# Performance work log

Hardware: AMD Instinct MI355X
Metric: run time of the kernel (lower is better)

Reference implementation:

```python
import jax, jax.numpy as jnp
import numpy as np

N = 100000   # nodes
E = 1600000  # edges
B = 128      # graphs
VOCAB, EMB, HID = 10000, 128, 128


def gcn_conv(x, src, dst, ew, W, b, n_nodes):
    # PyG GCNConv: x' = D^{-1/2}(A_w + I) D^{-1/2} (x W) + b, self-loop weight 1
    x = x @ W  # [N, H]
    loop = jnp.arange(n_nodes)
    src2 = jnp.concatenate([src, loop])
    dst2 = jnp.concatenate([dst, loop])
    ew2 = jnp.concatenate([ew, jnp.ones((n_nodes,), x.dtype)])
    deg = jax.ops.segment_sum(ew2, dst2, num_segments=n_nodes)
    dinv = jnp.where(deg > 0, deg ** -0.5, 0.0)
    norm = dinv[src2] * ew2 * dinv[dst2]                      # [E+N]
    msg = x[src2] * norm[:, None]                             # gather-scale
    out = jax.ops.segment_sum(msg, dst2, num_segments=n_nodes)  # scatter-add
    return out + b


def setup_inputs() -> dict:
    key = jax.random.key(0)
    ks = jax.random.split(key, 12)
    x_idx = jax.random.randint(ks[0], (N,), 0, VOCAB)
    edge_index = jax.random.randint(ks[1], (2, E), 0, N)
    edge_weight = jax.random.uniform(ks[2], (E,), jnp.float32)
    batch = jnp.sort(jax.random.randint(ks[3], (N,), 0, B))
    emb_table = jax.random.normal(ks[4], (VOCAB, EMB), jnp.float32)
    emb_table = emb_table.at[0].set(0.0)  # padding_idx=0
    s = 1.0 / np.sqrt(EMB)
    W1 = jax.random.uniform(ks[5], (EMB, HID), jnp.float32, -s, s)
    b1 = jnp.zeros((HID,), jnp.float32)
    W2 = jax.random.uniform(ks[6], (HID, HID), jnp.float32, -s, s)
    b2 = jnp.zeros((HID,), jnp.float32)
    mlp_W1 = jax.random.uniform(ks[7], (HID, HID // 2), jnp.float32, -s, s)
    mlp_b1 = jax.random.uniform(ks[8], (HID // 2,), jnp.float32, -s, s)
    s2 = 1.0 / np.sqrt(HID // 2)
    mlp_W2 = jax.random.uniform(ks[9], (HID // 2, 2), jnp.float32, -s2, s2)
    mlp_b2 = jax.random.uniform(ks[10], (2,), jnp.float32, -s2, s2)
    return dict(x_idx=x_idx, edge_index=edge_index, edge_weight=edge_weight,
                batch=batch, emb_table=emb_table, W1=W1, b1=b1, W2=W2, b2=b2,
                mlp_W1=mlp_W1, mlp_b1=mlp_b1, mlp_W2=mlp_W2, mlp_b2=mlp_b2)


def reference(x_idx, edge_index, edge_weight, batch, emb_table, W1, b1, W2, b2,
              mlp_W1, mlp_b1, mlp_W2, mlp_b2):
    src, dst = edge_index[0], edge_index[1]
    x = emb_table[x_idx]                                  # embedding lookup
    x = jax.nn.relu(gcn_conv(x, src, dst, edge_weight, W1, b1, N))
    # dropout is inference no-op
    x = jax.nn.relu(gcn_conv(x, src, dst, edge_weight, W2, b2, N))
    # global mean pool over graphs
    sums = jax.ops.segment_sum(x, batch, num_segments=B)
    cnts = jax.ops.segment_sum(jnp.ones((N,), x.dtype), batch, num_segments=B)
    g = sums / jnp.maximum(cnts, 1.0)[:, None]            # [B, HID]
    h = jax.nn.relu(g @ mlp_W1 + mlp_b1)
    out = h @ mlp_W2 + mlp_b2
    return jax.nn.softmax(out, axis=1)
```

## Files before the change

### kernel.cpp

```cpp
#include <hip/hip_runtime.h>
#include <hip/hip_bf16.h>

#define NN 100000
#define NE 1600000
#define NB 128
#define NV 10000
#define HD 128

#define NBUCK 782
#define EBLK 512
#define EPB (NE / EBLK)

using bf16x8 = __attribute__((ext_vector_type(8))) short;
using f32x4  = __attribute__((ext_vector_type(4))) float;
typedef __attribute__((ext_vector_type(8))) unsigned short ushortv8;
typedef __attribute__((ext_vector_type(8))) unsigned char ucharv8;
typedef float f32x2 __attribute__((ext_vector_type(2)));

__device__ __forceinline__ float bf2f(unsigned short b) {
  return __uint_as_float((unsigned)b << 16);
}
__device__ __forceinline__ unsigned short f2bf(float f) {
  __hip_bfloat16 h = __float2bfloat16(f);
  return *reinterpret_cast<unsigned short*>(&h);
}
__device__ __forceinline__ unsigned char f2fp8(float f) {
  return (unsigned char)(__builtin_amdgcn_cvt_pk_fp8_f32(f, 0.f, 0, false) & 0xff);
}
__device__ __forceinline__ unsigned packSN(unsigned s, float v) {
  return (s << 15) | ((unsigned)f2bf(v) & 0x7fffu);
}
__device__ __forceinline__ float unpackN(unsigned u) {
  return __uint_as_float((u & 0x7fffu) << 16);
}
__device__ __forceinline__ void acc16(float* acc, uint4 u, float c) {
  f32x2 v;
  v = __builtin_amdgcn_cvt_pk_f32_fp8((int)u.x, false); acc[0] += c*v[0]; acc[1] += c*v[1];
  v = __builtin_amdgcn_cvt_pk_f32_fp8((int)u.x, true);  acc[2] += c*v[0]; acc[3] += c*v[1];
  v = __builtin_amdgcn_cvt_pk_f32_fp8((int)u.y, false); acc[4] += c*v[0]; acc[5] += c*v[1];
  v = __builtin_amdgcn_cvt_pk_f32_fp8((int)u.y, true);  acc[6] += c*v[0]; acc[7] += c*v[1];
  v = __builtin_amdgcn_cvt_pk_f32_fp8((int)u.z, false); acc[8] += c*v[0]; acc[9] += c*v[1];
  v = __builtin_amdgcn_cvt_pk_f32_fp8((int)u.z, true);  acc[10]+= c*v[0]; acc[11]+= c*v[1];
  v = __builtin_amdgcn_cvt_pk_f32_fp8((int)u.w, false); acc[12]+= c*v[0]; acc[13]+= c*v[1];
  v = __builtin_amdgcn_cvt_pk_f32_fp8((int)u.w, true);  acc[14]+= c*v[0]; acc[15]+= c*v[1];
}


__global__ __launch_bounds__(1024) void k_bcount(const int* __restrict__ dst,
                                                 int* __restrict__ cntmat) {
  __shared__ int h[NBUCK];
  int t = threadIdx.x, blk = blockIdx.x;
  for (int i = t; i < NBUCK; i += 1024) h[i] = 0;
  __syncthreads();
  int base = blk * EPB;
  for (int i = t; i < EPB; i += 1024) atomicAdd(&h[dst[base + i] >> 7], 1);
  __syncthreads();
  for (int i = t; i < NBUCK; i += 1024) cntmat[(size_t)blk * NBUCK + i] = h[i];
}

__global__ __launch_bounds__(256) void k_cscan(int* __restrict__ cntmat,
                                               int* __restrict__ totals) {
  __shared__ int sh[256];
  int bu = blockIdx.x, t = threadIdx.x;
  int v0 = cntmat[(size_t)(2 * t) * NBUCK + bu];
  int v1 = cntmat[(size_t)(2 * t + 1) * NBUCK + bu];
  int s = v0 + v1;
  sh[t] = s;
  __syncthreads();
  #pragma unroll
  for (int off = 1; off < 256; off <<= 1) {
    int u = (t >= off) ? sh[t - off] : 0;
    __syncthreads();
    sh[t] += u;
    __syncthreads();
  }
  int pre = sh[t] - s;
  cntmat[(size_t)(2 * t) * NBUCK + bu] = pre;
  cntmat[(size_t)(2 * t + 1) * NBUCK + bu] = pre + v0;
  if (t == 255) totals[bu] = sh[255];
}

__global__ __launch_bounds__(1024) void k_tscan(const int* __restrict__ totals,
                                                int* __restrict__ bucketBase) {
  __shared__ int sh[1024];
  int t = threadIdx.x;
  int v = (t < NBUCK) ? totals[t] : 0;
  sh[t] = v;
  __syncthreads();
  #pragma unroll
  for (int off = 1; off < 1024; off <<= 1) {
    int u = (t >= off) ? sh[t - off] : 0;
    __syncthreads();
    sh[t] += u;
    __syncthreads();
  }
  if (t < NBUCK) bucketBase[t] = sh[t] - v;
  if (t == NBUCK - 1) bucketBase[NBUCK] = sh[t];
}

__global__ __launch_bounds__(1024) void k_bscatter(const int* __restrict__ src,
                                                   const int* __restrict__ dst,
                                                   const float* __restrict__ ew,
                                                   const int* __restrict__ cntmat,
                                                   const int* __restrict__ bucketBase,
                                                   uint2* __restrict__ spair) {
  __shared__ int off[NBUCK];
  int t = threadIdx.x, blk = blockIdx.x;
  for (int i = t; i < NBUCK; i += 1024)
    off[i] = bucketBase[i] + cntmat[(size_t)blk * NBUCK + i];
  __syncthreads();
  int base = blk * EPB;
  for (int i = t; i < EPB; i += 1024) {
    int e = base + i;
    int d = dst[e];
    unsigned pew = packSN((unsigned)src[e], ew[e]);
    int pos = atomicAdd(&off[d >> 7], 1);
    spair[pos] = make_uint2(pew, (unsigned)(d & 127));
  }
}

__global__ __launch_bounds__(256) void k_bdeg(const uint2* __restrict__ spair,
                                              const int* __restrict__ bucketBase,
                                              int* __restrict__ rowptr,
                                              float* __restrict__ dinv) {
  __shared__ int cnt[128];
  __shared__ float ws[128];
  __shared__ int sh[128];
  int bu = blockIdx.x, t = threadIdx.x;
  if (t < 128) { cnt[t] = 0; ws[t] = 0.f; }
  __syncthreads();
  int ebeg = bucketBase[bu], eend = bucketBase[bu + 1];
  for (int e = ebeg + t; e < eend; e += 256) {
    uint2 p = spair[e];
    atomicAdd(&cnt[p.y], 1);
    atomicAdd(&ws[p.y], unpackN(p.x));
  }
  __syncthreads();
  int v = 0;
  if (t < 128) { v = cnt[t]; sh[t] = v; }
  __syncthreads();
  #pragma unroll
  for (int off = 1; off < 128; off <<= 1) {
    int u = 0;
    if (t < 128 && t >= off) u = sh[t - off];
    __syncthreads();
    if (t < 128) sh[t] += u;
    __syncthreads();
  }
  if (t < 128) {
    int gid = (bu << 7) + t;
    if (gid < NN) {
      rowptr[gid] = ebeg + sh[t] - v;
      dinv[gid] = rsqrtf(1.0f + ws[t]);
    }
    if (gid == NN) rowptr[NN] = NE;
  }
}

__global__ __launch_bounds__(256) void k_bfill(const uint2* __restrict__ spair,
                                               const int* __restrict__ bucketBase,
                                               const int* __restrict__ rowptr,
                                               const float* __restrict__ dinv,
                                               unsigned* __restrict__ csr) {
  __shared__ int cnt[128];
  __shared__ float sdv[128];
  __shared__ int srp[128];
  int bu = blockIdx.x, t = threadIdx.x;
  if (t < 128) {
    cnt[t] = 0;
    int gid = (bu << 7) + t;
    if (gid < NN) { sdv[t] = dinv[gid]; srp[t] = rowptr[gid]; }
  }
  __syncthreads();
  int ebeg = bucketBase[bu], eend = bucketBase[bu + 1];
  for (int e = ebeg + t; e < eend; e += 256) {
    uint2 p = spair[e];
    int dl = (int)p.y;
    unsigned s = p.x >> 15;
    float ewf = unpackN(p.x);
    int r = atomicAdd(&cnt[dl], 1);
    float nrm = dinv[s] * ewf * sdv[dl];
    csr[srp[dl] + r] = packSN(s, nrm);
  }
}

__global__ void k_wprep2(const float* __restrict__ W1, const float* __restrict__ W2,
                         unsigned short* __restrict__ Wt1, unsigned short* __restrict__ Wt2) {
  int t = blockIdx.x * blockDim.x + threadIdx.x;
  const float* W = (t < 16384) ? W1 : W2;
  unsigned short* Wt = (t < 16384) ? Wt1 : Wt2;
  int i = t & 16383;
  int k = i >> 7, n = i & 127;
  Wt[n * 128 + k] = f2bf(W[k * 128 + n]);
}

template <bool AF32>
__global__ __launch_bounds__(256) void k_gemm_mfma(const void* __restrict__ Av,
                                                   const unsigned short* __restrict__ Wt,
                                                   unsigned char* __restrict__ C, int M) {
  __shared__ unsigned char Cs[128][132];
  const int t = threadIdx.x;
  const int wave = t >> 6, lane = t & 63;
  const int lrow = lane & 15, lk = lane >> 4;
  const int row0 = blockIdx.x * 128;
  const int wrow = row0 + wave * 32;

  f32x4 acc[2][8];
  #pragma unroll
  for (int i = 0; i < 2; ++i)
    #pragma unroll
    for (int j = 0; j < 8; ++j) acc[i][j] = (f32x4){0.f, 0.f, 0.f, 0.f};

  #pragma unroll
  for (int kt = 0; kt < 4; ++kt) {
    bf16x8 a[2];
    #pragma unroll
    for (int rt = 0; rt < 2; ++rt) {
      int r = wrow + rt * 16 + lrow;
      bf16x8 av = (bf16x8){0, 0, 0, 0, 0, 0, 0, 0};
      if (r < M) {
        if (AF32) {
          const float* ap = (const float*)Av + (size_t)r * HD + kt * 32 + lk * 8;
          #pragma unroll
          for (int j = 0; j < 8; ++j) av[j] = (short)f2bf(ap[j]);
        } else {
          av = *(const bf16x8*)((const unsigned short*)Av + (size_t)r * HD + kt * 32 + lk * 8);
        }
      }
      a[rt] = av;
    }
    #pragma unroll
    for (int ct = 0; ct < 8; ++ct) {
      bf16x8 b = *(const bf16x8*)(Wt + (size_t)(ct * 16 + lrow) * HD + kt * 32 + lk * 8);
      acc[0][ct] = __builtin_amdgcn_mfma_f32_16x16x32_bf16(a[0], b, acc[0][ct], 0, 0, 0);
      acc[1][ct] = __builtin_amdgcn_mfma_f32_16x16x32_bf16(a[1], b, acc[1][ct], 0, 0, 0);
    }
  }

  #pragma unroll
  for (int rt = 0; rt < 2; ++rt)
    #pragma unroll
    for (int ct = 0; ct < 8; ++ct)
      #pragma unroll
      for (int reg = 0; reg < 4; ++reg) {
        int lr = wave * 32 + rt * 16 + lk * 4 + reg;
        Cs[lr][ct * 16 + lrow] = f2fp8(acc[rt][ct][reg]);
      }
  __syncthreads();

  #pragma unroll
  for (int i = 0; i < 8; ++i) {
    int idx = t + i * 256;
    int r = idx >> 4;
    int c = (idx & 15) * 8;
    int gr = row0 + r;
    if (gr < M)
      *(ucharv8*)(C + (size_t)gr * HD + c) = *(const ucharv8*)&Cs[r][c];
  }
}

template <bool IND, bool POOL>
__global__ __launch_bounds__(256) void k_agg8(const unsigned char* __restrict__ xw,
                                              const int* __restrict__ xidx,
                                              const int* __restrict__ rowptr,
                                              const unsigned* __restrict__ csr,
                                              const float* __restrict__ dinv,
                                              const float* __restrict__ bias,
                                              unsigned short* __restrict__ outp,
                                              const int* __restrict__ batch,
                                              float* __restrict__ sums) {
  int t = threadIdx.x;
  int n = blockIdx.x * 32 + (t >> 3);
  int lane = t & 7;
  int beg = rowptr[n], end = rowptr[n + 1];

  int sn = IND ? xidx[n] : n;
  uint4 uself = *(const uint4*)(xw + (size_t)sn * HD + lane * 16);

  float acc[16];
  #pragma unroll
  for (int j = 0; j < 16; ++j) acc[j] = 0.f;

  int e = beg;
  int alignEnd = min(end, (beg + 3) & ~3);
  for (; e < alignEnd; ++e) {
    unsigned u = csr[e];
    int s0 = (int)(u >> 15);
    if (IND) s0 = xidx[s0];
    float c0 = unpackN(u);
    uint4 u0 = *(const uint4*)(xw + (size_t)s0 * HD + lane * 16);
    acc16(acc, u0, c0);
  }
  for (; e + 3 < end; e += 4) {
    uint4 q = *(const uint4*)(csr + e);
    int s0 = (int)(q.x >> 15), s1 = (int)(q.y >> 15);
    int s2 = (int)(q.z >> 15), s3 = (int)(q.w >> 15);
    if (IND) { s0 = xidx[s0]; s1 = xidx[s1]; s2 = xidx[s2]; s3 = xidx[s3]; }
    float c0 = unpackN(q.x), c1 = unpackN(q.y);
    float c2 = unpackN(q.z), c3 = unpackN(q.w);
    uint4 u0 = *(const uint4*)(xw + (size_t)s0 * HD + lane * 16);
    uint4 u1 = *(const uint4*)(xw + (size_t)s1 * HD + lane * 16);
    uint4 u2 = *(const uint4*)(xw + (size_t)s2 * HD + lane * 16);
    uint4 u3 = *(const uint4*)(xw + (size_t)s3 * HD + lane * 16);
    acc16(acc, u0, c0); acc16(acc, u1, c1);
    acc16(acc, u2, c2); acc16(acc, u3, c3);
  }
  for (; e < end; ++e) {
    unsigned u = csr[e];
    int s0 = (int)(u >> 15);
    if (IND) s0 = xidx[s0];
    float c0 = unpackN(u);
    uint4 u0 = *(const uint4*)(xw + (size_t)s0 * HD + lane * 16);
    acc16(acc, u0, c0);
  }

  float d = dinv[n];
  acc16(acc, uself, d * d);

  const float4* bp = reinterpret_cast<const float4*>(bias + lane * 16);
  float4 b0 = bp[0], b1 = bp[1], b2 = bp[2], b3 = bp[3];
  float o[16];
  o[0]  = fmaxf(acc[0]  + b0.x, 0.f); o[1]  = fmaxf(acc[1]  + b0.y, 0.f);
  o[2]  = fmaxf(acc[2]  + b0.z, 0.f); o[3]  = fmaxf(acc[3]  + b0.w, 0.f);
  o[4]  = fmaxf(acc[4]  + b1.x, 0.f); o[5]  = fmaxf(acc[5]  + b1.y, 0.f);
  o[6]  = fmaxf(acc[6]  + b1.z, 0.f); o[7]  = fmaxf(acc[7]  + b1.w, 0.f);
  o[8]  = fmaxf(acc[8]  + b2.x, 0.f); o[9]  = fmaxf(acc[9]  + b2.y, 0.f);
  o[10] = fmaxf(acc[10] + b2.z, 0.f); o[11] = fmaxf(acc[11] + b2.w, 0.f);
  o[12] = fmaxf(acc[12] + b3.x, 0.f); o[13] = fmaxf(acc[13] + b3.y, 0.f);
  o[14] = fmaxf(acc[14] + b3.z, 0.f); o[15] = fmaxf(acc[15] + b3.w, 0.f);

  if constexpr (!POOL) {
    ushortv8 r0, r1;
    #pragma unroll
    for (int j = 0; j < 8; ++j) { r0[j] = f2bf(o[j]); r1[j] = f2bf(o[8 + j]); }
    *(ushortv8*)(outp + (size_t)n * HD + lane * 16) = r0;
    *(ushortv8*)(outp + (size_t)n * HD + lane * 16 + 8) = r1;
  } else {
    __shared__ float pool[32][129];
    __shared__ int ib[32];
    int nl = t >> 3;
    #pragma unroll
    for (int j = 0; j < 16; ++j) pool[nl][lane * 16 + j] = o[j];
    if (t < 32) ib[t] = batch[blockIdx.x * 32 + t];
    __syncthreads();
    if (t < 128) {
      float a = 0.f;
      int c = t;
      #pragma unroll 4
      for (int i = 0; i < 32; ++i) {
        a += pool[i][c];
        if (i == 31 || ib[i + 1] != ib[i]) {
          atomicAdd(&sums[(size_t)ib[i] * HD + c], a);
          a = 0.f;
        }
      }
    }
  }
}

__global__ __launch_bounds__(256) void k_zero_counts(float* __restrict__ sums,
                                                     const int* __restrict__ batch,
                                                     float* __restrict__ cnt) {
  int i = blockIdx.x * blockDim.x + threadIdx.x;
  if (i < NB * HD) sums[i] = 0.f;
  if (blockIdx.x == 0 && threadIdx.x < NB) {
    int b = threadIdx.x;
    auto lb = [&](int v) {
      int lo = 0, hi = NN;
      while (lo < hi) { int m = (lo + hi) >> 1; if (batch[m] < v) lo = m + 1; else hi = m; }
      return lo;
    };
    cnt[b] = (float)(lb(b + 1) - lb(b));
  }
}

__global__ __launch_bounds__(64) void k_head(const float* __restrict__ sums,
                                             const float* __restrict__ cnt,
                                             const float* __restrict__ W1,
                                             const float* __restrict__ b1,
                                             const float* __restrict__ W2,
                                             const float* __restrict__ b2,
                                             float* __restrict__ out) {
  int g = blockIdx.x, t = threadIdx.x;
  __shared__ float gv[128];
  __shared__ float h[64];
  __shared__ float logits[2];
  float c = fmaxf(cnt[g], 1.0f);
  gv[t] = sums[g * HD + t] / c;
  gv[t + 64] = sums[g * HD + 64 + t] / c;
  __syncthreads();
  float acc = b1[t];
  for (int k = 0; k < 128; ++k) acc += gv[k] * W1[k * 64 + t];
  h[t] = fmaxf(acc, 0.f);
  __syncthreads();
  if (t < 2) {
    float a = b2[t];
    for (int j = 0; j < 64; ++j) a += h[j] * W2[j * 2 + t];
    logits[t] = a;
  }
  __syncthreads();
  if (t < 2) {
    float m = fmaxf(logits[0], logits[1]);
    float e0 = __expf(logits[0] - m), e1 = __expf(logits[1] - m);
    out[g * 2 + t] = (t == 0 ? e0 : e1) / (e0 + e1);
  }
}

extern "C" void kernel_launch(void* const* d_in, const int* in_sizes, int n_in,
                              void* d_out, int out_size, void* d_ws, size_t ws_size,
                              hipStream_t stream) {
  const int*   x_idx = (const int*)d_in[0];
  const int*   eidx  = (const int*)d_in[1];
  const float* ew    = (const float*)d_in[2];
  const int*   batch = (const int*)d_in[3];
  const float* emb   = (const float*)d_in[4];
  const float* W1    = (const float*)d_in[5];
  const float* b1    = (const float*)d_in[6];
  const float* W2    = (const float*)d_in[7];
  const float* b2    = (const float*)d_in[8];
  const float* mW1   = (const float*)d_in[9];
  const float* mb1   = (const float*)d_in[10];
  const float* mW2   = (const float*)d_in[11];
  const float* mb2   = (const float*)d_in[12];
  const int* src = eidx;
  const int* dst = eidx + NE;
  float* out = (float*)d_out;

  char* ws = (char*)d_ws;
  size_t off = 0;
  auto alloc = [&](size_t bytes) {
    void* p = ws + off;
    off += (bytes + 255) & ~(size_t)255;
    return p;
  };
  int*   cntmat     = (int*)alloc((size_t)EBLK * NBUCK * 4);
  int*   totals     = (int*)alloc((size_t)NBUCK * 4);
  int*   bucketBase = (int*)alloc((size_t)(NBUCK + 1) * 4);
  int*   rowptr     = (int*)alloc((size_t)(NN + 1) * 4);
  float* dinv       = (float*)alloc((size_t)NN * 4);
  unsigned* csr     = (unsigned*)alloc((size_t)NE * 4);
  unsigned short* Wt1  = (unsigned short*)alloc((size_t)HD * HD * 2);
  unsigned short* Wt2  = (unsigned short*)alloc((size_t)HD * HD * 2);
  unsigned char* embW  = (unsigned char*)alloc((size_t)NV * HD);
  unsigned char* bufA  = (unsigned char*)alloc((size_t)NN * HD);
  float* sums    = (float*)alloc((size_t)NB * HD * 4);
  float* cnt     = (float*)alloc((size_t)NB * 4);
  char* unionReg = (char*)alloc((size_t)NN * HD * 2);
  uint2* spair = (uint2*)unionReg;
  unsigned short* bufB = (unsigned short*)unionReg;

  k_bcount<<<EBLK, 1024, 0, stream>>>(dst, cntmat);
  k_cscan<<<NBUCK, 256, 0, stream>>>(cntmat, totals);
  k_tscan<<<1, 1024, 0, stream>>>(totals, bucketBase);
  k_bscatter<<<EBLK, 1024, 0, stream>>>(src, dst, ew, cntmat, bucketBase, spair);
  k_bdeg<<<NBUCK, 256, 0, stream>>>(spair, bucketBase, rowptr, dinv);
  k_bfill<<<NBUCK, 256, 0, stream>>>(spair, bucketBase, rowptr, dinv, csr);

  k_wprep2<<<128, 256, 0, stream>>>(W1, W2, Wt1, Wt2);

  k_gemm_mfma<true><<<(NV + 127) / 128, 256, 0, stream>>>(emb, Wt1, embW, NV);

  k_zero_counts<<<64, 256, 0, stream>>>(sums, batch, cnt);

  k_agg8<true, false><<<NN / 32, 256, 0, stream>>>(
      embW, x_idx, rowptr, csr, dinv, b1, bufB, nullptr, nullptr);

  k_gemm_mfma<false><<<(NN + 127) / 128, 256, 0, stream>>>(bufB, Wt2, bufA, NN);
  k_agg8<false, true><<<NN / 32, 256, 0, stream>>>(
      bufA, nullptr, rowptr, csr, dinv, b2, nullptr, batch, sums);

  k_head<<<NB, 64, 0, stream>>>(sums, cnt, mW1, mb1, mW2, mb2, out);
}
```

Baseline: 198.6 us.

## Precompute vocab-indexed CSR for layer 1 and unroll gather loop by eight

The CSR fill kernel now writes a second CSR array whose source ids are already mapped through x_idx. The first aggregation pass can then gather embedding rows directly, without a dependent xidx load per edge. The aggregation inner loop is unrolled from four to eight edges to keep more gathers in flight, and the pooling shared array is padded to 132 columns. This costs an extra 6.4MB write plus an xidx lookup per edge in the fill kernel, and adds register pressure from the wider unroll.

```diff
diff --git a/kernel.cpp b/kernel.cpp
--- a/kernel.cpp
+++ b/kernel.cpp
@@ -161,7 +161,9 @@
                                                const int* __restrict__ bucketBase,
                                                const int* __restrict__ rowptr,
                                                const float* __restrict__ dinv,
-                                               unsigned* __restrict__ csr) {
+                                               const int* __restrict__ xidx,
+                                               unsigned* __restrict__ csrS,
+                                               unsigned* __restrict__ csrV) {
   __shared__ int cnt[128];
   __shared__ float sdv[128];
   __shared__ int srp[128];
@@ -180,7 +182,9 @@
     float ewf = unpackN(p.x);
     int r = atomicAdd(&cnt[dl], 1);
     float nrm = dinv[s] * ewf * sdv[dl];
-    csr[srp[dl] + r] = packSN(s, nrm);
+    int pos = srp[dl] + r;
+    csrS[pos] = packSN(s, nrm);
+    csrV[pos] = packSN((unsigned)xidx[s], nrm);
   }
 }
 
@@ -259,7 +263,7 @@
   }
 }
 
-template <bool IND, bool POOL>
+template <bool SELFIND, bool POOL>
 __global__ __launch_bounds__(256) void k_agg8(const unsigned char* __restrict__ xw,
                                               const int* __restrict__ xidx,
                                               const int* __restrict__ rowptr,
@@ -274,7 +278,7 @@
   int lane = t & 7;
   int beg = rowptr[n], end = rowptr[n + 1];
 
-  int sn = IND ? xidx[n] : n;
+  int sn = SELFIND ? xidx[n] : n;
   uint4 uself = *(const uint4*)(xw + (size_t)sn * HD + lane * 16);
 
   float acc[16];
@@ -286,29 +290,45 @@
   for (; e < alignEnd; ++e) {
     unsigned u = csr[e];
     int s0 = (int)(u >> 15);
-    if (IND) s0 = xidx[s0];
     float c0 = unpackN(u);
     uint4 u0 = *(const uint4*)(xw + (size_t)s0 * HD + lane * 16);
     acc16(acc, u0, c0);
   }
-  for (; e + 3 < end; e += 4) {
-    uint4 q = *(const uint4*)(csr + e);
-    int s0 = (int)(q.x >> 15), s1 = (int)(q.y >> 15);
-    int s2 = (int)(q.z >> 15), s3 = (int)(q.w >> 15);
-    if (IND) { s0 = xidx[s0]; s1 = xidx[s1]; s2 = xidx[s2]; s3 = xidx[s3]; }
-    float c0 = unpackN(q.x), c1 = unpackN(q.y);
-    float c2 = unpackN(q.z), c3 = unpackN(q.w);
+  for (; e + 7 < end; e += 8) {
+    uint4 qa = *(const uint4*)(csr + e);
+    uint4 qb = *(const uint4*)(csr + e + 4);
+    int s0 = (int)(qa.x >> 15), s1 = (int)(qa.y >> 15);
+    int s2 = (int)(qa.z >> 15), s3 = (int)(qa.w >> 15);
+    int s4 = (int)(qb.x >> 15), s5 = (int)(qb.y >> 15);
+    int s6 = (int)(qb.z >> 15), s7 = (int)(qb.w >> 15);
     uint4 u0 = *(const uint4*)(xw + (size_t)s0 * HD + lane * 16);
     uint4 u1 = *(const uint4*)(xw + (size_t)s1 * HD + lane * 16);
     uint4 u2 = *(const uint4*)(xw + (size_t)s2 * HD + lane * 16);
     uint4 u3 = *(const uint4*)(xw + (size_t)s3 * HD + lane * 16);
-    acc16(acc, u0, c0); acc16(acc, u1, c1);
-    acc16(acc, u2, c2); acc16(acc, u3, c3);
+    uint4 u4 = *(const uint4*)(xw + (size_t)s4 * HD + lane * 16);
+    uint4 u5 = *(const uint4*)(xw + (size_t)s5 * HD + lane * 16);
+    uint4 u6 = *(const uint4*)(xw + (size_t)s6 * HD + lane * 16);
+    uint4 u7 = *(const uint4*)(xw + (size_t)s7 * HD + lane * 16);
+    acc16(acc, u0, unpackN(qa.x)); acc16(acc, u1, unpackN(qa.y));
+    acc16(acc, u2, unpackN(qa.z)); acc16(acc, u3, unpackN(qa.w));
+    acc16(acc, u4, unpackN(qb.x)); acc16(acc, u5, unpackN(qb.y));
+    acc16(acc, u6, unpackN(qb.z)); acc16(acc, u7, unpackN(qb.w));
+  }
+  if (e + 3 < end) {
+    uint4 q = *(const uint4*)(csr + e);
+    int s0 = (int)(q.x >> 15), s1 = (int)(q.y >> 15);
+    int s2 = (int)(q.z >> 15), s3 = (int)(q.w >> 15);
+    uint4 u0 = *(const uint4*)(xw + (size_t)s0 * HD + lane * 16);
+    uint4 u1 = *(const uint4*)(xw + (size_t)s1 * HD + lane * 16);
+    uint4 u2 = *(const uint4*)(xw + (size_t)s2 * HD + lane * 16);
+    uint4 u3 = *(const uint4*)(xw + (size_t)s3 * HD + lane * 16);
+    acc16(acc, u0, unpackN(q.x)); acc16(acc, u1, unpackN(q.y));
+    acc16(acc, u2, unpackN(q.z)); acc16(acc, u3, unpackN(q.w));
+    e += 4;
   }
   for (; e < end; ++e) {
     unsigned u = csr[e];
     int s0 = (int)(u >> 15);
-    if (IND) s0 = xidx[s0];
     float c0 = unpackN(u);
     uint4 u0 = *(const uint4*)(xw + (size_t)s0 * HD + lane * 16);
     acc16(acc, u0, c0);
@@ -336,7 +356,7 @@
     *(ushortv8*)(outp + (size_t)n * HD + lane * 16) = r0;
     *(ushortv8*)(outp + (size_t)n * HD + lane * 16 + 8) = r1;
   } else {
-    __shared__ float pool[32][129];
+    __shared__ float pool[32][132];
     __shared__ int ib[32];
     int nl = t >> 3;
     #pragma unroll
@@ -438,7 +458,8 @@
   int*   bucketBase = (int*)alloc((size_t)(NBUCK + 1) * 4);
   int*   rowptr     = (int*)alloc((size_t)(NN + 1) * 4);
   float* dinv       = (float*)alloc((size_t)NN * 4);
-  unsigned* csr     = (unsigned*)alloc((size_t)NE * 4);
+  unsigned* csrS    = (unsigned*)alloc((size_t)NE * 4);
+  unsigned* csrV    = (unsigned*)alloc((size_t)NE * 4);
   unsigned short* Wt1  = (unsigned short*)alloc((size_t)HD * HD * 2);
   unsigned short* Wt2  = (unsigned short*)alloc((size_t)HD * HD * 2);
   unsigned char* embW  = (unsigned char*)alloc((size_t)NV * HD);
@@ -454,7 +475,7 @@
   k_tscan<<<1, 1024, 0, stream>>>(totals, bucketBase);
   k_bscatter<<<EBLK, 1024, 0, stream>>>(src, dst, ew, cntmat, bucketBase, spair);
   k_bdeg<<<NBUCK, 256, 0, stream>>>(spair, bucketBase, rowptr, dinv);
-  k_bfill<<<NBUCK, 256, 0, stream>>>(spair, bucketBase, rowptr, dinv, csr);
+  k_bfill<<<NBUCK, 256, 0, stream>>>(spair, bucketBase, rowptr, dinv, x_idx, csrS, csrV);
 
   k_wprep2<<<128, 256, 0, stream>>>(W1, W2, Wt1, Wt2);
 
@@ -463,11 +484,11 @@
   k_zero_counts<<<64, 256, 0, stream>>>(sums, batch, cnt);
 
   k_agg8<true, false><<<NN / 32, 256, 0, stream>>>(
-      embW, x_idx, rowptr, csr, dinv, b1, bufB, nullptr, nullptr);
+      embW, x_idx, rowptr, csrV, dinv, b1, bufB, nullptr, nullptr);
 
   k_gemm_mfma<false><<<(NN + 127) / 128, 256, 0, stream>>>(bufB, Wt2, bufA, NN);
   k_agg8<false, true><<<NN / 32, 256, 0, stream>>>(
-      bufA, nullptr, rowptr, csr, dinv, b2, nullptr, batch, sums);
+      bufA, nullptr, rowptr, csrS, dinv, b2, nullptr, batch, sums);
 
   k_head<<<NB, 64, 0, stream>>>(sums, cnt, mW1, mb1, mW2, mb2, out);
 }
```

Result: slower. 220.9 us (+11.2%).

## Pre-translate CSR source indices to vocab ids and prefetch next edge quad

Applied to the files above, without the earlier changes.

Adds a kernel that rewrites the CSR source fields into embedding-vocab indices once, so the first aggregation no longer does a dependent xidx lookup per edge before gathering. The first layer uses this translated CSR and the second layer uses the original one. The quad loop is also restructured to load the next four CSR entries before processing the current four, giving software prefetch. The cost is an extra kernel pass over 1.6M edges and an extra 6.4MB buffer. It also assumes vocab ids fit in the 17-bit source field.

```diff
diff --git a/kernel.cpp b/kernel.cpp
--- a/kernel.cpp
+++ b/kernel.cpp
@@ -181,6 +181,16 @@
     int r = atomicAdd(&cnt[dl], 1);
     float nrm = dinv[s] * ewf * sdv[dl];
     csr[srp[dl] + r] = packSN(s, nrm);
+  }
+}
+
+__global__ void k_trans(const unsigned* __restrict__ csrS,
+                        const int* __restrict__ xidx,
+                        unsigned* __restrict__ csrV) {
+  int i = blockIdx.x * blockDim.x + threadIdx.x;
+  if (i < NE) {
+    unsigned u = csrS[i];
+    csrV[i] = ((unsigned)xidx[u >> 15] << 15) | (u & 0x7fffu);
   }
 }
 
@@ -259,7 +269,7 @@
   }
 }
 
-template <bool IND, bool POOL>
+template <bool SELFIND, bool POOL>
 __global__ __launch_bounds__(256) void k_agg8(const unsigned char* __restrict__ xw,
                                               const int* __restrict__ xidx,
                                               const int* __restrict__ rowptr,
@@ -274,41 +284,47 @@
   int lane = t & 7;
   int beg = rowptr[n], end = rowptr[n + 1];
 
-  int sn = IND ? xidx[n] : n;
+  int sn = SELFIND ? xidx[n] : n;
   uint4 uself = *(const uint4*)(xw + (size_t)sn * HD + lane * 16);
 
   float acc[16];
   #pragma unroll
   for (int j = 0; j < 16; ++j) acc[j] = 0.f;
+
+  auto quad = [&](uint4 q) {
+    int s0 = (int)(q.x >> 15), s1 = (int)(q.y >> 15);
+    int s2 = (int)(q.z >> 15), s3 = (int)(q.w >> 15);
+    uint4 u0 = *(const uint4*)(xw + (size_t)s0 * HD + lane * 16);
+    uint4 u1 = *(const uint4*)(xw + (size_t)s1 * HD + lane * 16);
+    uint4 u2 = *(const uint4*)(xw + (size_t)s2 * HD + lane * 16);
+    uint4 u3 = *(const uint4*)(xw + (size_t)s3 * HD + lane * 16);
+    acc16(acc, u0, unpackN(q.x)); acc16(acc, u1, unpackN(q.y));
+    acc16(acc, u2, unpackN(q.z)); acc16(acc, u3, unpackN(q.w));
+  };
 
   int e = beg;
   int alignEnd = min(end, (beg + 3) & ~3);
   for (; e < alignEnd; ++e) {
     unsigned u = csr[e];
     int s0 = (int)(u >> 15);
-    if (IND) s0 = xidx[s0];
     float c0 = unpackN(u);
     uint4 u0 = *(const uint4*)(xw + (size_t)s0 * HD + lane * 16);
     acc16(acc, u0, c0);
   }
-  for (; e + 3 < end; e += 4) {
+  int nquad = (end - e) >> 2;
+  if (nquad > 0) {
     uint4 q = *(const uint4*)(csr + e);
-    int s0 = (int)(q.x >> 15), s1 = (int)(q.y >> 15);
-    int s2 = (int)(q.z >> 15), s3 = (int)(q.w >> 15);
-    if (IND) { s0 = xidx[s0]; s1 = xidx[s1]; s2 = xidx[s2]; s3 = xidx[s3]; }
-    float c0 = unpackN(q.x), c1 = unpackN(q.y);
-    float c2 = unpackN(q.z), c3 = unpackN(q.w);
-    uint4 u0 = *(const uint4*)(xw + (size_t)s0 * HD + lane * 16);
-    uint4 u1 = *(const uint4*)(xw + (size_t)s1 * HD + lane * 16);
-    uint4 u2 = *(const uint4*)(xw + (size_t)s2 * HD + lane * 16);
-    uint4 u3 = *(const uint4*)(xw + (size_t)s3 * HD + lane * 16);
-    acc16(acc, u0, c0); acc16(acc, u1, c1);
-    acc16(acc, u2, c2); acc16(acc, u3, c3);
+    for (int i = 1; i < nquad; ++i) {
+      uint4 qn = *(const uint4*)(csr + e + 4 * i);
+      quad(q);
+      q = qn;
+    }
+    quad(q);
+    e += nquad * 4;
   }
   for (; e < end; ++e) {
     unsigned u = csr[e];
     int s0 = (int)(u >> 15);
-    if (IND) s0 = xidx[s0];
     float c0 = unpackN(u);
     uint4 u0 = *(const uint4*)(xw + (size_t)s0 * HD + lane * 16);
     acc16(acc, u0, c0);
@@ -438,7 +454,8 @@
   int*   bucketBase = (int*)alloc((size_t)(NBUCK + 1) * 4);
   int*   rowptr     = (int*)alloc((size_t)(NN + 1) * 4);
   float* dinv       = (float*)alloc((size_t)NN * 4);
-  unsigned* csr     = (unsigned*)alloc((size_t)NE * 4);
+  unsigned* csrS    = (unsigned*)alloc((size_t)NE * 4);
+  unsigned* csrV    = (unsigned*)alloc((size_t)NE * 4);
   unsigned short* Wt1  = (unsigned short*)alloc((size_t)HD * HD * 2);
   unsigned short* Wt2  = (unsigned short*)alloc((size_t)HD * HD * 2);
   unsigned char* embW  = (unsigned char*)alloc((size_t)NV * HD);
@@ -454,7 +471,8 @@
   k_tscan<<<1, 1024, 0, stream>>>(totals, bucketBase);
   k_bscatter<<<EBLK, 1024, 0, stream>>>(src, dst, ew, cntmat, bucketBase, spair);
   k_bdeg<<<NBUCK, 256, 0, stream>>>(spair, bucketBase, rowptr, dinv);
-  k_bfill<<<NBUCK, 256, 0, stream>>>(spair, bucketBase, rowptr, dinv, csr);
+  k_bfill<<<NBUCK, 256, 0, stream>>>(spair, bucketBase, rowptr, dinv, csrS);
+  k_trans<<<(NE + 255) / 256, 256, 0, stream>>>(csrS, x_idx, csrV);
 
   k_wprep2<<<128, 256, 0, stream>>>(W1, W2, Wt1, Wt2);
 
@@ -463,11 +481,11 @@
   k_zero_counts<<<64, 256, 0, stream>>>(sums, batch, cnt);
 
   k_agg8<true, false><<<NN / 32, 256, 0, stream>>>(
-      embW, x_idx, rowptr, csr, dinv, b1, bufB, nullptr, nullptr);
+      embW, x_idx, rowptr, csrV, dinv, b1, bufB, nullptr, nullptr);
 
   k_gemm_mfma<false><<<(NN + 127) / 128, 256, 0, stream>>>(bufB, Wt2, bufA, NN);
   k_agg8<false, true><<<NN / 32, 256, 0, stream>>>(
-      bufA, nullptr, rowptr, csr, dinv, b2, nullptr, batch, sums);
+      bufA, nullptr, rowptr, csrS, dinv, b2, nullptr, batch, sums);
 
   k_head<<<NB, 64, 0, stream>>>(sums, cnt, mW1, mb1, mW2, mb2, out);
 }
```

New measurement: 194.1 us. 2.2% less time.
